# Kernel optimization log

Measured on AMD Instinct MI355X. Metric: run time of the kernel, lower is better.

Reference implementation:

```python
import jax, jax.numpy as jnp
import numpy as np

N_NODES = 50000
N_EDGES = 800000
D_IN = 64
D_HID = 64
D_OUT = 64


def setup_inputs() -> dict:
    key = jax.random.key(0)
    ks = jax.random.split(key, 6)
    X = jax.random.normal(ks[0], (N_NODES, D_IN), dtype=jnp.float32)
    edge_index = jax.random.randint(ks[1], (2, N_EDGES), 0, N_NODES, dtype=jnp.int64)
    edge_weight = jax.random.uniform(ks[2], (N_EDGES,), dtype=jnp.float32)
    W1 = jax.random.normal(ks[3], (D_IN, D_HID), dtype=jnp.float32) / np.float32(np.sqrt(D_IN))
    b1 = jnp.zeros((D_HID,), dtype=jnp.float32)
    W2 = jax.random.normal(ks[4], (D_HID, D_OUT), dtype=jnp.float32) / np.float32(np.sqrt(D_HID))
    b2 = jnp.zeros((D_OUT,), dtype=jnp.float32)
    return {"X": X, "edge_weight": edge_weight, "W1": W1, "b1": b1,
            "W2": W2, "b2": b2, "edge_index": edge_index}


def reference(X, edge_weight, W1, b1, W2, b2, edge_index):
    # conv(A, X) = (A @ X) @ W + b with sparse A given as (edge_index, edge_weight)
    src = edge_index[0]
    dst = edge_index[1]

    def agg(H):
        # weighted neighborhood sum: [E, d] messages scattered to [N, d]
        msgs = edge_weight[:, None] * H[src]
        return jax.ops.segment_sum(msgs, dst, num_segments=N_NODES)

    # layer 1: conv -> relu (dropout p=0 is identity)
    H = jax.nn.relu(agg(X) @ W1 + b1)
    # last layer: conv, no final activation (l_act=None)
    return agg(H) @ W2 + b2
```

## Files before the change

kernel.cpp:

```cpp
#include <hip/hip_runtime.h>

#define D 64

template <bool PRE>
__global__ __launch_bounds__(256, 4) void gemm64_kernel(
    const float* __restrict__ A, const float* __restrict__ W,
    const float* __restrict__ bpre, float* __restrict__ out, int N) {
  __shared__ float sA[64][68];
  __shared__ float sW[64][68];
  const int t = threadIdx.x;
  const int rowBase = blockIdx.x * 64;

#pragma unroll
  for (int i = t * 4; i < 4096; i += 1024) {
    const int k = i >> 6, c = i & 63;
    *reinterpret_cast<float4*>(&sW[k][c]) =
        *reinterpret_cast<const float4*>(W + i);
  }
#pragma unroll
  for (int i = t * 4; i < 4096; i += 1024) {
    const int r = i >> 6, k = i & 63;
    const int row = rowBase + r;
    float4 a = make_float4(0.f, 0.f, 0.f, 0.f);
    if (row < N) a = *reinterpret_cast<const float4*>(A + (size_t)row * D + k);
    if (PRE) {
      const float4 b = *reinterpret_cast<const float4*>(bpre + k);
      a.x = fmaxf(a.x + b.x, 0.f);
      a.y = fmaxf(a.y + b.y, 0.f);
      a.z = fmaxf(a.z + b.z, 0.f);
      a.w = fmaxf(a.w + b.w, 0.f);
    }
    *reinterpret_cast<float4*>(&sA[r][k]) = a;
  }
  __syncthreads();

  const int ty = t >> 4, tx = t & 15;
  float4 acc0 = make_float4(0.f, 0.f, 0.f, 0.f);
  float4 acc1 = make_float4(0.f, 0.f, 0.f, 0.f);
  float4 acc2 = make_float4(0.f, 0.f, 0.f, 0.f);
  float4 acc3 = make_float4(0.f, 0.f, 0.f, 0.f);

#pragma unroll 4
  for (int kq = 0; kq < 16; ++kq) {
    const float4 w0 = *reinterpret_cast<const float4*>(&sW[kq * 4 + 0][tx * 4]);
    const float4 w1 = *reinterpret_cast<const float4*>(&sW[kq * 4 + 1][tx * 4]);
    const float4 w2 = *reinterpret_cast<const float4*>(&sW[kq * 4 + 2][tx * 4]);
    const float4 w3 = *reinterpret_cast<const float4*>(&sW[kq * 4 + 3][tx * 4]);
    const float4 a0 = *reinterpret_cast<const float4*>(&sA[ty * 4 + 0][kq * 4]);
    const float4 a1 = *reinterpret_cast<const float4*>(&sA[ty * 4 + 1][kq * 4]);
    const float4 a2 = *reinterpret_cast<const float4*>(&sA[ty * 4 + 2][kq * 4]);
    const float4 a3 = *reinterpret_cast<const float4*>(&sA[ty * 4 + 3][kq * 4]);
#define FMA4(ACC, AV)                                                     \
    ACC.x += AV.x * w0.x + AV.y * w1.x + AV.z * w2.x + AV.w * w3.x;       \
    ACC.y += AV.x * w0.y + AV.y * w1.y + AV.z * w2.y + AV.w * w3.y;       \
    ACC.z += AV.x * w0.z + AV.y * w1.z + AV.z * w2.z + AV.w * w3.z;       \
    ACC.w += AV.x * w0.w + AV.y * w1.w + AV.z * w2.w + AV.w * w3.w;
    FMA4(acc0, a0) FMA4(acc1, a1) FMA4(acc2, a2) FMA4(acc3, a3)
#undef FMA4
  }

  const int row0 = rowBase + ty * 4;
  if (row0 + 0 < N) *reinterpret_cast<float4*>(out + (size_t)(row0 + 0) * D + tx * 4) = acc0;
  if (row0 + 1 < N) *reinterpret_cast<float4*>(out + (size_t)(row0 + 1) * D + tx * 4) = acc1;
  if (row0 + 2 < N) *reinterpret_cast<float4*>(out + (size_t)(row0 + 2) * D + tx * 4) = acc2;
  if (row0 + 3 < N) *reinterpret_cast<float4*>(out + (size_t)(row0 + 3) * D + tx * 4) = acc3;
}

__global__ __launch_bounds__(256) void hist_kernel(
    const int* __restrict__ dst, int* __restrict__ deg,
    int* __restrict__ posw, int E) {
  int e = blockIdx.x * 256 + threadIdx.x;
  if (e < E) posw[e] = atomicAdd(&deg[dst[e]], 1);
}

#define SCAN_CHUNK 1024
__global__ __launch_bounds__(256) void scan_part_kernel(
    const int* __restrict__ deg, int* __restrict__ offs,
    int* __restrict__ bsums, int N) {
  __shared__ int s[256];
  const int t = threadIdx.x;
  const int base = blockIdx.x * SCAN_CHUNK + t * 4;
  int v0 = 0, v1 = 0, v2 = 0, v3 = 0;
  if (base + 3 < N) {
    const int4 v = *reinterpret_cast<const int4*>(deg + base);
    v0 = v.x; v1 = v.y; v2 = v.z; v3 = v.w;
  } else {
    if (base + 0 < N) v0 = deg[base + 0];
    if (base + 1 < N) v1 = deg[base + 1];
    if (base + 2 < N) v2 = deg[base + 2];
  }
  const int tsum = v0 + v1 + v2 + v3;
  s[t] = tsum;
  __syncthreads();
  for (int off = 1; off < 256; off <<= 1) {
    int x = (t >= off) ? s[t - off] : 0;
    __syncthreads();
    s[t] += x;
    __syncthreads();
  }
  const int excl = s[t] - tsum;
  if (base + 0 < N) offs[base + 0] = excl;
  if (base + 1 < N) offs[base + 1] = excl + v0;
  if (base + 2 < N) offs[base + 2] = excl + v0 + v1;
  if (base + 3 < N) offs[base + 3] = excl + v0 + v1 + v2;
  if (t == 255) bsums[blockIdx.x] = s[255];
}

__global__ __launch_bounds__(1024) void scan_sums_kernel(
    int* __restrict__ bsums, int* __restrict__ offsN, int nb) {
  __shared__ int s[1024];
  const int t = threadIdx.x;
  const int v = (t < nb) ? bsums[t] : 0;
  s[t] = v;
  __syncthreads();
  for (int off = 1; off < 1024; off <<= 1) {
    int x = (t >= off) ? s[t - off] : 0;
    __syncthreads();
    s[t] += x;
    __syncthreads();
  }
  if (t < nb) bsums[t] = s[t] - v;
  if (t == nb - 1) *offsN = s[t];
}

__global__ __launch_bounds__(256) void scan_add_kernel(
    int* __restrict__ offs, const int* __restrict__ bsums, int N) {
  const int i = blockIdx.x * 256 + threadIdx.x;
  if (i < N) offs[i] += bsums[i >> 10];
}

__global__ __launch_bounds__(256) void bucket_kernel(
    const int* __restrict__ src, const int* __restrict__ dst,
    const float* __restrict__ ew, const int* __restrict__ offs,
    const int* __restrict__ posw, int2* __restrict__ pairs, int E) {
  int e = blockIdx.x * 256 + threadIdx.x;
  if (e < E) {
    const int pos = offs[dst[e]] + posw[e];
    pairs[pos] = make_int2(src[e], __float_as_int(ew[e]));
  }
}

#define NB 256
#define RB 256

__global__ __launch_bounds__(256) void p1_hist_kernel(
    const int* __restrict__ dst, int* __restrict__ countsT, int E, int epb) {
  __shared__ int h[RB];
  const int t = threadIdx.x;
  h[t] = 0;
  __syncthreads();
  const int base = blockIdx.x * epb;
  const int lim = min(base + epb, E);
  for (int i = base + t; i < lim; i += 256) atomicAdd(&h[dst[i] >> 8], 1);
  __syncthreads();
  countsT[t * NB + blockIdx.x] = h[t];
}

__global__ __launch_bounds__(256) void p1_scatter_kernel(
    const int* __restrict__ src, const int* __restrict__ dst,
    const float* __restrict__ ew, const int* __restrict__ SC,
    const int* __restrict__ bsums, int2* __restrict__ tmp, int E, int epb) {
  __shared__ int cur[RB];
  const int t = threadIdx.x;
  const int idx = t * NB + blockIdx.x;
  cur[t] = SC[idx] + bsums[idx >> 10];
  __syncthreads();
  const int base = blockIdx.x * epb;
  const int lim = min(base + epb, E);
  for (int i = base + t; i < lim; i += 256) {
    const int d = dst[i];
    const unsigned s = (unsigned)src[i];
    const float w = ew[i];
    const int pos = atomicAdd(&cur[d >> 8], 1);
    tmp[pos] = make_int2((int)((unsigned)d | (s << 16)), __float_as_int(w));
  }
}

__global__ __launch_bounds__(256) void p2_kernel(
    const int2* __restrict__ tmp, const int* __restrict__ SC,
    const int* __restrict__ bsums,
    int* __restrict__ offs, int2* __restrict__ pairs, int N, int E) {
  __shared__ int h[RB];
  __shared__ int s[RB];
  __shared__ int cur[RB];
  const int t = threadIdx.x;
  const int b = blockIdx.x;
  const int segBeg = SC[b * RB] + bsums[b >> 2];
  const int segEnd = (b == RB - 1) ? E : (SC[(b + 1) * RB] + bsums[(b + 1) >> 2]);

  h[t] = 0;
  __syncthreads();
  for (int i = segBeg + t; i < segEnd; i += 256)
    atomicAdd(&h[tmp[i].x & 255], 1);
  __syncthreads();

  const int v = h[t];
  s[t] = v;
  __syncthreads();
  for (int off = 1; off < 256; off <<= 1) {
    int x = (t >= off) ? s[t - off] : 0;
    __syncthreads();
    s[t] += x;
    __syncthreads();
  }
  const int excl = s[t] - v;
  cur[t] = segBeg + excl;
  const int node = b * RB + t;
  if (node <= N) offs[node] = segBeg + excl;
  __syncthreads();

  for (int i = segBeg + t; i < segEnd; i += 256) {
    const int2 r = tmp[i];
    const int lo = r.x & 255;
    const int pos = atomicAdd(&cur[lo], 1);
    pairs[pos] = make_int2((int)(((unsigned)r.x) >> 16), r.y);
  }
}

template <bool BIAS>
__global__ __launch_bounds__(256) void gather_agg_kernel(
    const float* __restrict__ H, const int* __restrict__ offs,
    const int2* __restrict__ pairs,
    const float* __restrict__ bias, float* __restrict__ out, int N) {
  const int l4 = threadIdx.x & 15;
  const int node = blockIdx.x * 16 + (threadIdx.x >> 4);
  if (node >= N) return;
  const int beg = offs[node], end = offs[node + 1];
  float4 A0 = make_float4(0.f, 0.f, 0.f, 0.f);
  float4 A1 = make_float4(0.f, 0.f, 0.f, 0.f);
  int i = beg;
  for (; i + 2 <= end; i += 2) {
    const int2 p0 = pairs[i], p1 = pairs[i + 1];
    const float4 v0 = *reinterpret_cast<const float4*>(H + (size_t)p0.x * D + l4 * 4);
    const float4 v1 = *reinterpret_cast<const float4*>(H + (size_t)p1.x * D + l4 * 4);
    const float w0 = __int_as_float(p0.y), w1 = __int_as_float(p1.y);
    A0.x += w0 * v0.x; A0.y += w0 * v0.y; A0.z += w0 * v0.z; A0.w += w0 * v0.w;
    A1.x += w1 * v1.x; A1.y += w1 * v1.y; A1.z += w1 * v1.z; A1.w += w1 * v1.w;
  }
  if (i < end) {
    const int2 p = pairs[i];
    const float4 v = *reinterpret_cast<const float4*>(H + (size_t)p.x * D + l4 * 4);
    const float w = __int_as_float(p.y);
    A0.x += w * v.x; A0.y += w * v.y; A0.z += w * v.z; A0.w += w * v.w;
  }
  float4 r;
  r.x = A0.x + A1.x; r.y = A0.y + A1.y; r.z = A0.z + A1.z; r.w = A0.w + A1.w;
  if (BIAS) {
    const float4 b = *reinterpret_cast<const float4*>(bias + l4 * 4);
    r.x += b.x; r.y += b.y; r.z += b.z; r.w += b.w;
  }
  *reinterpret_cast<float4*>(out + (size_t)node * D + l4 * 4) = r;
}

__global__ __launch_bounds__(256) void scatter_kernel(
    const float* __restrict__ H, const float* __restrict__ ew,
    const int* __restrict__ src, const int* __restrict__ dst,
    float* __restrict__ out, int nEdges) {
  const int tid = blockIdx.x * 256 + threadIdx.x;
  const int e = tid >> 4;
  if (e >= nEdges) return;
  const int c = (tid & 15) * 4;
  const float w = ew[e];
  const float4 v = *reinterpret_cast<const float4*>(H + (size_t)src[e] * D + c);
  float* o = out + (size_t)dst[e] * D + c;
  atomicAdd(o + 0, w * v.x);
  atomicAdd(o + 1, w * v.y);
  atomicAdd(o + 2, w * v.z);
  atomicAdd(o + 3, w * v.w);
}

__global__ __launch_bounds__(256) void fill_bias_kernel(
    float* __restrict__ out, const float* __restrict__ b, int total) {
  int i = blockIdx.x * 256 + threadIdx.x;
  if (i < total) out[i] = b[i & 63];
}

extern "C" void kernel_launch(void* const* d_in, const int* in_sizes, int n_in,
                              void* d_out, int out_size, void* d_ws,
                              size_t ws_size, hipStream_t stream) {
  const float* X  = (const float*)d_in[0];
  const float* ew = (const float*)d_in[1];
  const float* W1 = (const float*)d_in[2];
  const float* b1 = (const float*)d_in[3];
  const float* W2 = (const float*)d_in[4];
  const float* b2 = (const float*)d_in[5];
  const int*   ei = (const int*)d_in[6];

  const int N = in_sizes[0] / D;
  const int E = in_sizes[6] / 2;
  const int* src = ei;
  const int* dst = ei + E;
  float* out = (float*)d_out;

  char* ws = (char*)d_ws;
  float* buf0 = (float*)ws;                 ws += (size_t)N * D * 4;
  float* buf1 = (float*)ws;                 ws += (size_t)N * D * 4;
  const size_t baseBytes = (size_t)(ws - (char*)d_ws);
  int2*  pairs  = (int2*)ws;                ws += (size_t)E * 8;
  int*   offs   = (int*)ws;                 ws += (size_t)(N + 1) * 4;
  const size_t needBytes = (size_t)(ws - (char*)d_ws);

  const int gemmBlocks = (N + 63) / 64;
  const int aggBlocks  = (N + 15) / 16;
  const int edgeBlocks = (E + 255) / 256;

  if (ws_size >= needBytes) {
    if (N <= 65536 && (size_t)N * D * 4 >= (size_t)(2 * NB * RB + 1 + 64) * 4 &&
        (size_t)N * D * 4 >= (size_t)E * 8) {
      int*  countsT = (int*)buf0;
      int*  SC      = (int*)buf0 + NB * RB;
      int*  bsums   = (int*)buf0 + 2 * NB * RB + 1;
      int2* tmp     = (int2*)buf1;

      const int epb = (E + NB - 1) / NB;
      p1_hist_kernel<<<NB, 256, 0, stream>>>(dst, countsT, E, epb);
      scan_part_kernel<<<NB * RB / SCAN_CHUNK, 256, 0, stream>>>(countsT, SC, bsums, NB * RB);
      scan_sums_kernel<<<1, 1024, 0, stream>>>(bsums, SC + NB * RB, NB * RB / SCAN_CHUNK);
      p1_scatter_kernel<<<NB, 256, 0, stream>>>(src, dst, ew, SC, bsums, tmp, E, epb);
      p2_kernel<<<RB, 256, 0, stream>>>(tmp, SC, bsums, offs, pairs, N, E);
    } else {
      int* deg   = (int*)buf0;
      int* bsums = (int*)buf0 + N;
      int* posw  = (int*)buf1;
      const int nb = (N + SCAN_CHUNK - 1) / SCAN_CHUNK;
      hipMemsetAsync(deg, 0, (size_t)N * 4, stream);
      hist_kernel<<<edgeBlocks, 256, 0, stream>>>(dst, deg, posw, E);
      scan_part_kernel<<<nb, 256, 0, stream>>>(deg, offs, bsums, N);
      scan_sums_kernel<<<1, 1024, 0, stream>>>(bsums, offs + N, nb);
      scan_add_kernel<<<(N + 255) / 256, 256, 0, stream>>>(offs, bsums, N);
      bucket_kernel<<<edgeBlocks, 256, 0, stream>>>(src, dst, ew, offs, posw, pairs, E);
    }

    gemm64_kernel<false><<<gemmBlocks, 256, 0, stream>>>(X, W1, nullptr, buf0, N);
    gather_agg_kernel<false><<<aggBlocks, 256, 0, stream>>>(buf0, offs, pairs, nullptr, buf1, N);
    gemm64_kernel<true><<<gemmBlocks, 256, 0, stream>>>(buf1, W2, b1, buf0, N);
    gather_agg_kernel<true><<<aggBlocks, 256, 0, stream>>>(buf0, offs, pairs, b2, out, N);
  } else if (ws_size >= baseBytes) {
    const int scatBlocks = (E * 16 + 255) / 256;
    const int fillBlocks = (N * D + 255) / 256;
    gemm64_kernel<false><<<gemmBlocks, 256, 0, stream>>>(X, W1, nullptr, buf0, N);
    hipMemsetAsync(buf1, 0, (size_t)N * D * 4, stream);
    scatter_kernel<<<scatBlocks, 256, 0, stream>>>(buf0, ew, src, dst, buf1, E);
    gemm64_kernel<true><<<gemmBlocks, 256, 0, stream>>>(buf1, W2, b1, buf0, N);
    fill_bias_kernel<<<fillBlocks, 256, 0, stream>>>(out, b2, N * D);
    scatter_kernel<<<scatBlocks, 256, 0, stream>>>(buf0, ew, src, dst, out, E);
  }
}
```

Baseline: 124.1 us.

## Fuse first-layer aggregation with bias, ReLU and second GEMM in one kernel

```diff
diff --git a/kernel.cpp b/kernel.cpp
--- a/kernel.cpp
+++ b/kernel.cpp
@@ -66,6 +66,97 @@
   if (row0 + 3 < N) *reinterpret_cast<float4*>(out + (size_t)(row0 + 3) * D + tx * 4) = acc3;
 }
 
+__global__ __launch_bounds__(256, 4) void agg_gemm_kernel(
+    const float* __restrict__ H, const int* __restrict__ offs,
+    const int2* __restrict__ pairs, const float* __restrict__ b1,
+    const float* __restrict__ W, float* __restrict__ out, int N) {
+  __shared__ float sA[64][68];
+  __shared__ float sW[64][68];
+  const int t = threadIdx.x;
+  const int rowBase = blockIdx.x * 64;
+
+#pragma unroll
+  for (int i = t * 4; i < 4096; i += 1024) {
+    const int k = i >> 6, c = i & 63;
+    *reinterpret_cast<float4*>(&sW[k][c]) =
+        *reinterpret_cast<const float4*>(W + i);
+  }
+
+  const int l4 = t & 15;
+  const int sub = t >> 4;
+  const float4 bb = *reinterpret_cast<const float4*>(b1 + l4 * 4);
+#pragma unroll
+  for (int p = 0; p < 4; ++p) {
+    const int r = p * 16 + sub;
+    const int node = rowBase + r;
+    float4 A0 = make_float4(0.f, 0.f, 0.f, 0.f);
+    float4 A1 = make_float4(0.f, 0.f, 0.f, 0.f);
+    float4 A2 = make_float4(0.f, 0.f, 0.f, 0.f);
+    float4 A3 = make_float4(0.f, 0.f, 0.f, 0.f);
+    if (node < N) {
+      const int beg = offs[node], end = offs[node + 1];
+      int i = beg;
+      for (; i + 4 <= end; i += 4) {
+        const int2 p0 = pairs[i], p1 = pairs[i + 1], p2 = pairs[i + 2], p3 = pairs[i + 3];
+        const float4 v0 = *reinterpret_cast<const float4*>(H + (size_t)p0.x * D + l4 * 4);
+        const float4 v1 = *reinterpret_cast<const float4*>(H + (size_t)p1.x * D + l4 * 4);
+        const float4 v2 = *reinterpret_cast<const float4*>(H + (size_t)p2.x * D + l4 * 4);
+        const float4 v3 = *reinterpret_cast<const float4*>(H + (size_t)p3.x * D + l4 * 4);
+        const float w0 = __int_as_float(p0.y), w1 = __int_as_float(p1.y);
+        const float w2 = __int_as_float(p2.y), w3 = __int_as_float(p3.y);
+        A0.x += w0 * v0.x; A0.y += w0 * v0.y; A0.z += w0 * v0.z; A0.w += w0 * v0.w;
+        A1.x += w1 * v1.x; A1.y += w1 * v1.y; A1.z += w1 * v1.z; A1.w += w1 * v1.w;
+        A2.x += w2 * v2.x; A2.y += w2 * v2.y; A2.z += w2 * v2.z; A2.w += w2 * v2.w;
+        A3.x += w3 * v3.x; A3.y += w3 * v3.y; A3.z += w3 * v3.z; A3.w += w3 * v3.w;
+      }
+      for (; i < end; ++i) {
+        const int2 pp = pairs[i];
+        const float4 v = *reinterpret_cast<const float4*>(H + (size_t)pp.x * D + l4 * 4);
+        const float w = __int_as_float(pp.y);
+        A0.x += w * v.x; A0.y += w * v.y; A0.z += w * v.z; A0.w += w * v.w;
+      }
+    }
+    float4 rr;
+    rr.x = fmaxf((A0.x + A1.x) + (A2.x + A3.x) + bb.x, 0.f);
+    rr.y = fmaxf((A0.y + A1.y) + (A2.y + A3.y) + bb.y, 0.f);
+    rr.z = fmaxf((A0.z + A1.z) + (A2.z + A3.z) + bb.z, 0.f);
+    rr.w = fmaxf((A0.w + A1.w) + (A2.w + A3.w) + bb.w, 0.f);
+    *reinterpret_cast<float4*>(&sA[r][l4 * 4]) = rr;
+  }
+  __syncthreads();
+
+  const int ty = t >> 4, tx = t & 15;
+  float4 acc0 = make_float4(0.f, 0.f, 0.f, 0.f);
+  float4 acc1 = make_float4(0.f, 0.f, 0.f, 0.f);
+  float4 acc2 = make_float4(0.f, 0.f, 0.f, 0.f);
+  float4 acc3 = make_float4(0.f, 0.f, 0.f, 0.f);
+
+#pragma unroll 4
+  for (int kq = 0; kq < 16; ++kq) {
+    const float4 w0 = *reinterpret_cast<const float4*>(&sW[kq * 4 + 0][tx * 4]);
+    const float4 w1 = *reinterpret_cast<const float4*>(&sW[kq * 4 + 1][tx * 4]);
+    const float4 w2 = *reinterpret_cast<const float4*>(&sW[kq * 4 + 2][tx * 4]);
+    const float4 w3 = *reinterpret_cast<const float4*>(&sW[kq * 4 + 3][tx * 4]);
+    const float4 a0 = *reinterpret_cast<const float4*>(&sA[ty * 4 + 0][kq * 4]);
+    const float4 a1 = *reinterpret_cast<const float4*>(&sA[ty * 4 + 1][kq * 4]);
+    const float4 a2 = *reinterpret_cast<const float4*>(&sA[ty * 4 + 2][kq * 4]);
+    const float4 a3 = *reinterpret_cast<const float4*>(&sA[ty * 4 + 3][kq * 4]);
+#define FMA4(ACC, AV)                                                     \
+    ACC.x += AV.x * w0.x + AV.y * w1.x + AV.z * w2.x + AV.w * w3.x;       \
+    ACC.y += AV.x * w0.y + AV.y * w1.y + AV.z * w2.y + AV.w * w3.y;       \
+    ACC.z += AV.x * w0.z + AV.y * w1.z + AV.z * w2.z + AV.w * w3.z;       \
+    ACC.w += AV.x * w0.w + AV.y * w1.w + AV.z * w2.w + AV.w * w3.w;
+    FMA4(acc0, a0) FMA4(acc1, a1) FMA4(acc2, a2) FMA4(acc3, a3)
+#undef FMA4
+  }
+
+  const int row0 = rowBase + ty * 4;
+  if (row0 + 0 < N) *reinterpret_cast<float4*>(out + (size_t)(row0 + 0) * D + tx * 4) = acc0;
+  if (row0 + 1 < N) *reinterpret_cast<float4*>(out + (size_t)(row0 + 1) * D + tx * 4) = acc1;
+  if (row0 + 2 < N) *reinterpret_cast<float4*>(out + (size_t)(row0 + 2) * D + tx * 4) = acc2;
+  if (row0 + 3 < N) *reinterpret_cast<float4*>(out + (size_t)(row0 + 3) * D + tx * 4) = acc3;
+}
+
 __global__ __launch_bounds__(256) void hist_kernel(
     const int* __restrict__ dst, int* __restrict__ deg,
     int* __restrict__ posw, int E) {
@@ -228,23 +319,33 @@
   const int beg = offs[node], end = offs[node + 1];
   float4 A0 = make_float4(0.f, 0.f, 0.f, 0.f);
   float4 A1 = make_float4(0.f, 0.f, 0.f, 0.f);
+  float4 A2 = make_float4(0.f, 0.f, 0.f, 0.f);
+  float4 A3 = make_float4(0.f, 0.f, 0.f, 0.f);
   int i = beg;
-  for (; i + 2 <= end; i += 2) {
-    const int2 p0 = pairs[i], p1 = pairs[i + 1];
+  for (; i + 4 <= end; i += 4) {
+    const int2 p0 = pairs[i], p1 = pairs[i + 1], p2 = pairs[i + 2], p3 = pairs[i + 3];
     const float4 v0 = *reinterpret_cast<const float4*>(H + (size_t)p0.x * D + l4 * 4);
     const float4 v1 = *reinterpret_cast<const float4*>(H + (size_t)p1.x * D + l4 * 4);
+    const float4 v2 = *reinterpret_cast<const float4*>(H + (size_t)p2.x * D + l4 * 4);
+    const float4 v3 = *reinterpret_cast<const float4*>(H + (size_t)p3.x * D + l4 * 4);
     const float w0 = __int_as_float(p0.y), w1 = __int_as_float(p1.y);
+    const float w2 = __int_as_float(p2.y), w3 = __int_as_float(p3.y);
     A0.x += w0 * v0.x; A0.y += w0 * v0.y; A0.z += w0 * v0.z; A0.w += w0 * v0.w;
     A1.x += w1 * v1.x; A1.y += w1 * v1.y; A1.z += w1 * v1.z; A1.w += w1 * v1.w;
-  }
-  if (i < end) {
+    A2.x += w2 * v2.x; A2.y += w2 * v2.y; A2.z += w2 * v2.z; A2.w += w2 * v2.w;
+    A3.x += w3 * v3.x; A3.y += w3 * v3.y; A3.z += w3 * v3.z; A3.w += w3 * v3.w;
+  }
+  for (; i < end; ++i) {
     const int2 p = pairs[i];
     const float4 v = *reinterpret_cast<const float4*>(H + (size_t)p.x * D + l4 * 4);
     const float w = __int_as_float(p.y);
     A0.x += w * v.x; A0.y += w * v.y; A0.z += w * v.z; A0.w += w * v.w;
   }
   float4 r;
-  r.x = A0.x + A1.x; r.y = A0.y + A1.y; r.z = A0.z + A1.z; r.w = A0.w + A1.w;
+  r.x = (A0.x + A1.x) + (A2.x + A3.x);
+  r.y = (A0.y + A1.y) + (A2.y + A3.y);
+  r.z = (A0.z + A1.z) + (A2.z + A3.z);
+  r.w = (A0.w + A1.w) + (A2.w + A3.w);
   if (BIAS) {
     const float4 b = *reinterpret_cast<const float4*>(bias + l4 * 4);
     r.x += b.x; r.y += b.y; r.z += b.z; r.w += b.w;
@@ -332,9 +433,8 @@
     }
 
     gemm64_kernel<false><<<gemmBlocks, 256, 0, stream>>>(X, W1, nullptr, buf0, N);
-    gather_agg_kernel<false><<<aggBlocks, 256, 0, stream>>>(buf0, offs, pairs, nullptr, buf1, N);
-    gemm64_kernel<true><<<gemmBlocks, 256, 0, stream>>>(buf1, W2, b1, buf0, N);
-    gather_agg_kernel<true><<<aggBlocks, 256, 0, stream>>>(buf0, offs, pairs, b2, out, N);
+    agg_gemm_kernel<<<gemmBlocks, 256, 0, stream>>>(buf0, offs, pairs, b1, W2, buf1, N);
+    gather_agg_kernel<true><<<aggBlocks, 256, 0, stream>>>(buf1, offs, pairs, b2, out, N);
   } else if (ws_size >= baseBytes) {
     const int scatBlocks = (E * 16 + 255) / 256;
     const int fillBlocks = (N * D + 255) / 256;
```

After: 117.2 us. 5.6% less time.
